# Kernel optimization log

Hardware: AMD Instinct MI355X
Metric: run time of the kernel (lower is better)

Reference implementation:

```python
import jax, jax.numpy as jnp
import numpy as np

B, S, D, H, L, C = 64, 2048, 64, 256, 2, 8  # batch, seq, input, hidden, layers, classes


def setup_inputs() -> dict:
    key = jax.random.key(0)
    ks = jax.random.split(key, 12)
    k = 1.0 / np.sqrt(H)  # torch LSTM/Linear init scale
    u = lambda kk, shape: jax.random.uniform(kk, shape, jnp.float32, -k, k)
    x = jax.random.normal(ks[0], (B, S, D), jnp.float32)
    lengths = jax.random.randint(ks[1], (B,), 1, S + 1).astype(jnp.int32)
    return {
        "x": x,
        "lengths": lengths,
        "Wih0": u(ks[2], (4 * H, D)),
        "Whh0": u(ks[3], (4 * H, H)),
        "bih0": u(ks[4], (4 * H,)),
        "bhh0": u(ks[5], (4 * H,)),
        "Wih1": u(ks[6], (4 * H, H)),
        "Whh1": u(ks[7], (4 * H, H)),
        "bih1": u(ks[8], (4 * H,)),
        "bhh1": u(ks[9], (4 * H,)),
        "Wfc": u(ks[10], (C, H)),
        "bfc": u(ks[11], (C,)),
    }


def _lstm_layer(x, Wih, Whh, bih, bhh):
    # x: [B,S,Din] -> h-sequence [B,S,H]; torch gate order i,f,g,o
    pre = jnp.einsum('bsd,gd->bsg', x, Wih) + bih + bhh  # [B,S,4H]
    Hh = Whh.shape[1]
    bsz = x.shape[0]

    def step(carry, p_t):
        h, c = carry
        gates = p_t + h @ Whh.T  # [B,4H]
        i, f, g, o = jnp.split(gates, 4, axis=-1)
        i = jax.nn.sigmoid(i)
        f = jax.nn.sigmoid(f)
        g = jnp.tanh(g)
        o = jax.nn.sigmoid(o)
        c = f * c + i * g
        h = o * jnp.tanh(c)
        return (h, c), h

    init = (jnp.zeros((bsz, Hh), x.dtype), jnp.zeros((bsz, Hh), x.dtype))
    _, hs = jax.lax.scan(step, init, jnp.swapaxes(pre, 0, 1))  # [S,B,H]
    return jnp.swapaxes(hs, 0, 1)


def reference(x, lengths, Wih0, Whh0, bih0, bhh0, Wih1, Whh1, bih1, bhh1, Wfc, bfc):
    h1 = _lstm_layer(x, Wih0, Whh0, bih0, bhh0)   # [B,S,H]
    h2 = _lstm_layer(h1, Wih1, Whh1, bih1, bhh1)  # [B,S,H]
    # pad_packed_sequence zeros outputs beyond each sequence's length
    valid = (jnp.arange(S)[None, :] < lengths[:, None])[..., None]  # [B,S,1]
    h2 = jnp.where(valid, h2, 0.0)
    emissions = jnp.einsum('bsh,ch->bsc', h2, Wfc) + bfc  # [B,S,C]
    return emissions
```

## Files before the change

kernel.cpp:

```cpp
#include <hip/hip_runtime.h>
#include <hip/hip_bf16.h>

#define BATCH 64
#define SEQ   2048
#define DIN   64
#define HID   256
#define NCLS  8

__device__ __forceinline__ float sigm(float x)  { return 1.0f / (1.0f + __expf(-x)); }
__device__ __forceinline__ float tanh_f(float x){ return 1.0f - 2.0f / (__expf(2.0f * x) + 1.0f); }

__global__ void init_out_kernel(float* __restrict__ out, const float* __restrict__ bfc) {
    int idx = blockIdx.x * blockDim.x + threadIdx.x;
    if (idx < BATCH * SEQ * NCLS) out[idx] = bfc[idx & 7];
}

__global__ void lstm_l0_kernel(
    const float* __restrict__ x,    const float* __restrict__ Wih0,
    const float* __restrict__ Whh0, const float* __restrict__ bih0,
    const float* __restrict__ bhh0, float* __restrict__ hist,
    int* __restrict__ flagsA)
{
    const int P   = blockIdx.x & 31;
    const int mem = blockIdx.x >> 5;
    const int tid = threadIdx.x;
    const int p   = tid >> 7;
    const int r   = tid & 127;
    const int row = (r >> 5) * 256 + mem * 32 + (r & 31);

    float w[40];
#pragma unroll
    for (int q = 0; q < 40; ++q) {
        int col = p * 40 + q;
        w[q] = (col < DIN) ? Wih0[row * DIN + col] : Whh0[row * HID + (col - DIN)];
    }
#pragma unroll
    for (int q = 0; q < 40; ++q) asm volatile("" : "+v"(w[q]));

    float biasv = 0.f;
    if (tid < 256) {
        int rr = tid & 127;
        int row2 = (rr >> 5) * 256 + mem * 32 + (rr & 31);
        biasv = bih0[row2] + bhh0[row2];
    }
    asm volatile("" : "+v"(biasv));
    float creg = 0.f;

    __shared__ __align__(16) float v[640];
    __shared__ float pbuf[2048];
    __shared__ float act[256];

    for (int t = 0; t < SEQ; ++t) {
        if (t > 0 && tid < 8) {
            while (__hip_atomic_load(&flagsA[P * 8 + tid], __ATOMIC_ACQUIRE,
                                     __HIP_MEMORY_SCOPE_AGENT) < t) {}
        }
        __syncthreads();
        if (tid < 640) {
            int n = (tid >= 320) ? 1 : 0;
            int j = tid - n * 320;
            int b = 2 * P + n;
            float val;
            if (j < DIN) {
                val = x[((size_t)b * SEQ + t) * DIN + j];
            } else {
                val = (t == 0) ? 0.f
                    : __hip_atomic_load(&hist[((size_t)(t - 1) * BATCH + b) * HID + (j - DIN)],
                                        __ATOMIC_RELAXED, __HIP_MEMORY_SCOPE_AGENT);
            }
            v[n * 320 + j] = val;
        }
        __syncthreads();

        float a0 = 0.f, a1 = 0.f;
#pragma unroll
        for (int qq = 0; qq < 10; ++qq) {
            float4 va = *(const float4*)&v[p * 40 + qq * 4];
            a0 = fmaf(w[qq * 4 + 0], va.x, a0);
            a0 = fmaf(w[qq * 4 + 1], va.y, a0);
            a0 = fmaf(w[qq * 4 + 2], va.z, a0);
            a0 = fmaf(w[qq * 4 + 3], va.w, a0);
            float4 vb = *(const float4*)&v[320 + p * 40 + qq * 4];
            a1 = fmaf(w[qq * 4 + 0], vb.x, a1);
            a1 = fmaf(w[qq * 4 + 1], vb.y, a1);
            a1 = fmaf(w[qq * 4 + 2], vb.z, a1);
            a1 = fmaf(w[qq * 4 + 3], vb.w, a1);
        }
        pbuf[p * 128 + r]        = a0;
        pbuf[1024 + p * 128 + r] = a1;
        __syncthreads();

        if (tid < 256) {
            int n = tid >> 7, rr = tid & 127;
            float s = biasv;
#pragma unroll
            for (int q = 0; q < 8; ++q) s += pbuf[n * 1024 + q * 128 + rr];
            act[n * 128 + rr] = ((rr >> 5) == 2) ? tanh_f(s) : sigm(s);
        }
        __syncthreads();

        if (tid < 64) {
            int n = tid >> 5, k = tid & 31, b = 2 * P + n;
            float iv = act[n * 128 + k],      fv = act[n * 128 + 32 + k];
            float gv = act[n * 128 + 64 + k], ov = act[n * 128 + 96 + k];
            creg = fv * creg + iv * gv;
            float h = ov * tanh_f(creg);
            __hip_atomic_store(&hist[((size_t)t * BATCH + b) * HID + mem * 32 + k],
                               h, __ATOMIC_RELAXED, __HIP_MEMORY_SCOPE_AGENT);
        }
        if (tid == 0) {
            __hip_atomic_store(&flagsA[P * 8 + mem], t + 1, __ATOMIC_RELEASE,
                               __HIP_MEMORY_SCOPE_AGENT);
        }
    }
}

__global__ void lstm_l1_kernel(
    const float* __restrict__ hist, const float* __restrict__ Wih1,
    const float* __restrict__ Whh1, const float* __restrict__ bih1,
    const float* __restrict__ bhh1, const float* __restrict__ Wfc,
    const float* __restrict__ bfc,  const int* __restrict__ lengths,
    float* __restrict__ out, float* __restrict__ xbuf, int* __restrict__ flagsB)
{
    const int g   = blockIdx.x & 15;
    const int mem = blockIdx.x >> 4;
    const int tid = threadIdx.x;
    const int p   = tid >> 6;
    const int r   = tid & 63;
    const int row = (r >> 4) * 256 + mem * 16 + (r & 15);

    float w[32];
#pragma unroll
    for (int q = 0; q < 32; ++q) {
        int col = p * 32 + q;
        w[q] = (col < HID) ? Wih1[row * HID + col] : Whh1[row * HID + (col - HID)];
    }
#pragma unroll
    for (int q = 0; q < 32; ++q) asm volatile("" : "+v"(w[q]));

    float biasv = 0.f;
    if (tid < 256) {
        int rr = tid & 63;
        int row2 = (rr >> 4) * 256 + mem * 16 + (rr & 15);
        biasv = bih1[row2] + bhh1[row2];
    }
    asm volatile("" : "+v"(biasv));
    float creg = 0.f;

    const int nf = mem & 3;
    const int c0 = (mem >> 2) * 2;
    float wfc = 0.f;
    if (tid < 512) wfc = Wfc[(c0 + (tid >> 8)) * HID + (tid & 255)];
    asm volatile("" : "+v"(wfc));
    const int  lenb = lengths[4 * g + nf];
    float bfcv = (tid < 2) ? bfc[c0 + tid] : 0.f;

    __shared__ __align__(16) float vbuf[2048];
    __shared__ float pbuf[4096];
    __shared__ float act[256];
    __shared__ float fcred[8];

    for (int t = 0; t < SEQ; ++t) {
        if (t > 0 && tid < 16) {
            while (__hip_atomic_load(&flagsB[g * 16 + tid], __ATOMIC_ACQUIRE,
                                     __HIP_MEMORY_SCOPE_AGENT) < t) {}
        }
        __syncthreads();
        {
            int n = tid >> 8, j = tid & 255, b = 4 * g + n;
            vbuf[n * 512 + j] = hist[((size_t)t * BATCH + b) * HID + j];
            float hv = (t == 0) ? 0.f
                : __hip_atomic_load(&xbuf[((size_t)b * 2 + ((t - 1) & 1)) * HID + j],
                                    __ATOMIC_RELAXED, __HIP_MEMORY_SCOPE_AGENT);
            vbuf[n * 512 + HID + j] = hv;
        }
        __syncthreads();

        float a0 = 0.f, a1 = 0.f, a2 = 0.f, a3 = 0.f;
#pragma unroll
        for (int qq = 0; qq < 8; ++qq) {
            float4 v0 = *(const float4*)&vbuf[p * 32 + qq * 4];
            a0 = fmaf(w[qq * 4 + 0], v0.x, a0); a0 = fmaf(w[qq * 4 + 1], v0.y, a0);
            a0 = fmaf(w[qq * 4 + 2], v0.z, a0); a0 = fmaf(w[qq * 4 + 3], v0.w, a0);
            float4 v1 = *(const float4*)&vbuf[512 + p * 32 + qq * 4];
            a1 = fmaf(w[qq * 4 + 0], v1.x, a1); a1 = fmaf(w[qq * 4 + 1], v1.y, a1);
            a1 = fmaf(w[qq * 4 + 2], v1.z, a1); a1 = fmaf(w[qq * 4 + 3], v1.w, a1);
            float4 v2 = *(const float4*)&vbuf[1024 + p * 32 + qq * 4];
            a2 = fmaf(w[qq * 4 + 0], v2.x, a2); a2 = fmaf(w[qq * 4 + 1], v2.y, a2);
            a2 = fmaf(w[qq * 4 + 2], v2.z, a2); a2 = fmaf(w[qq * 4 + 3], v2.w, a2);
            float4 v3 = *(const float4*)&vbuf[1536 + p * 32 + qq * 4];
            a3 = fmaf(w[qq * 4 + 0], v3.x, a3); a3 = fmaf(w[qq * 4 + 1], v3.y, a3);
            a3 = fmaf(w[qq * 4 + 2], v3.z, a3); a3 = fmaf(w[qq * 4 + 3], v3.w, a3);
        }
        pbuf[p * 64 + r]        = a0;
        pbuf[1024 + p * 64 + r] = a1;
        pbuf[2048 + p * 64 + r] = a2;
        pbuf[3072 + p * 64 + r] = a3;

        float fval = 0.f;
        if (t > 0 && tid < 512) {
            fval = vbuf[nf * 512 + HID + (tid & 255)] * wfc;
            fval += __shfl_xor(fval, 1);
            fval += __shfl_xor(fval, 2);
            fval += __shfl_xor(fval, 4);
            fval += __shfl_xor(fval, 8);
            fval += __shfl_xor(fval, 16);
            fval += __shfl_xor(fval, 32);
            if ((tid & 63) == 0) fcred[tid >> 6] = fval;
        }
        __syncthreads();

        if (tid < 256) {
            int n = tid >> 6, rw = tid & 63;
            float s = biasv;
#pragma unroll
            for (int q = 0; q < 16; ++q) s += pbuf[n * 1024 + q * 64 + rw];
            act[n * 64 + rw] = ((rw >> 4) == 2) ? tanh_f(s) : sigm(s);
        }
        if (t > 0 && tid < 2 && (t - 1) < lenb) {
            float s2 = fcred[tid * 4 + 0] + fcred[tid * 4 + 1]
                     + fcred[tid * 4 + 2] + fcred[tid * 4 + 3];
            out[((size_t)(4 * g + nf) * SEQ + (t - 1)) * NCLS + c0 + tid] = bfcv + s2;
        }
        __syncthreads();

        if (tid < 64) {
            int n = tid >> 4, k = tid & 15, b = 4 * g + n;
            float iv = act[n * 64 + k],      fv = act[n * 64 + 16 + k];
            float gv = act[n * 64 + 32 + k], ov = act[n * 64 + 48 + k];
            creg = fv * creg + iv * gv;
            float h = ov * tanh_f(creg);
            __hip_atomic_store(&xbuf[((size_t)b * 2 + (t & 1)) * HID + mem * 16 + k],
                               h, __ATOMIC_RELAXED, __HIP_MEMORY_SCOPE_AGENT);
        }
        if (tid == 0) {
            __hip_atomic_store(&flagsB[g * 16 + mem], t + 1, __ATOMIC_RELEASE,
                               __HIP_MEMORY_SCOPE_AGENT);
        }
    }

    if (tid < 16) {
        while (__hip_atomic_load(&flagsB[g * 16 + tid], __ATOMIC_ACQUIRE,
                                 __HIP_MEMORY_SCOPE_AGENT) < SEQ) {}
    }
    __syncthreads();
    float fval = 0.f;
    if (tid < 512) {
        int b = 4 * g + nf;
        float hv = __hip_atomic_load(&xbuf[((size_t)b * 2 + ((SEQ - 1) & 1)) * HID + (tid & 255)],
                                     __ATOMIC_RELAXED, __HIP_MEMORY_SCOPE_AGENT);
        fval = hv * wfc;
        fval += __shfl_xor(fval, 1);
        fval += __shfl_xor(fval, 2);
        fval += __shfl_xor(fval, 4);
        fval += __shfl_xor(fval, 8);
        fval += __shfl_xor(fval, 16);
        fval += __shfl_xor(fval, 32);
        if ((tid & 63) == 0) fcred[tid >> 6] = fval;
    }
    __syncthreads();
    if (tid < 2 && (SEQ - 1) < lenb) {
        float s2 = fcred[tid * 4 + 0] + fcred[tid * 4 + 1]
                 + fcred[tid * 4 + 2] + fcred[tid * 4 + 3];
        out[((size_t)(4 * g + nf) * SEQ + (SEQ - 1)) * NCLS + c0 + tid] = bfcv + s2;
    }
}

extern "C" void kernel_launch(void* const* d_in, const int* in_sizes, int n_in,
                              void* d_out, int out_size, void* d_ws, size_t ws_size,
                              hipStream_t stream) {
    (void)in_sizes; (void)n_in; (void)out_size;
    const float* x     = (const float*)d_in[0];
    const int*   lens  = (const int*)  d_in[1];
    const float* Wih0  = (const float*)d_in[2];
    const float* Whh0  = (const float*)d_in[3];
    const float* bih0  = (const float*)d_in[4];
    const float* bhh0  = (const float*)d_in[5];
    const float* Wih1  = (const float*)d_in[6];
    const float* Whh1  = (const float*)d_in[7];
    const float* bih1  = (const float*)d_in[8];
    const float* bhh1  = (const float*)d_in[9];
    const float* Wfc   = (const float*)d_in[10];
    const float* bfc   = (const float*)d_in[11];
    float* out = (float*)d_out;
    char*  ws  = (char*)d_ws;

    int*   flagsA = (int*)(ws);
    int*   flagsB = (int*)(ws + 1024);
    float* xbuf   = (float*)(ws + 2048);
    const size_t hist_off = 2048 + (size_t)BATCH * 2 * HID * 4;
    float* hist = (float*)(ws + hist_off);
    const size_t need = hist_off + (size_t)SEQ * BATCH * HID * 4;
    if (ws_size < need) return;

    hipMemsetAsync(ws, 0, hist_off, stream);
    init_out_kernel<<<(BATCH * SEQ * NCLS + 255) / 256, 256, 0, stream>>>(out, bfc);
    lstm_l0_kernel<<<256, 1024, 0, stream>>>(x, Wih0, Whh0, bih0, bhh0, hist, flagsA);
    lstm_l1_kernel<<<256, 1024, 0, stream>>>(hist, Wih1, Whh1, bih1, bhh1, Wfc, bfc,
                                             lens, out, xbuf, flagsB);
}
```

Measured before the change: 24.18 ms.

## Fuse both LSTM layers into one persistent kernel with wavefront pipelining

Result: slower. 30.66 ms (+26.8%).

```diff
diff --git a/kernel.cpp b/kernel.cpp
--- a/kernel.cpp
+++ b/kernel.cpp
@@ -10,196 +10,240 @@
 __device__ __forceinline__ float sigm(float x)  { return 1.0f / (1.0f + __expf(-x)); }
 __device__ __forceinline__ float tanh_f(float x){ return 1.0f - 2.0f / (__expf(2.0f * x) + 1.0f); }
 
+__device__ __forceinline__ void waitflag(int* f, int tgt) {
+    while (__hip_atomic_load(f, __ATOMIC_RELAXED, __HIP_MEMORY_SCOPE_AGENT) < tgt) {}
+    (void)__hip_atomic_load(f, __ATOMIC_ACQUIRE, __HIP_MEMORY_SCOPE_AGENT);
+}
+
 __global__ void init_out_kernel(float* __restrict__ out, const float* __restrict__ bfc) {
     int idx = blockIdx.x * blockDim.x + threadIdx.x;
     if (idx < BATCH * SEQ * NCLS) out[idx] = bfc[idx & 7];
 }
 
-__global__ void lstm_l0_kernel(
-    const float* __restrict__ x,    const float* __restrict__ Wih0,
-    const float* __restrict__ Whh0, const float* __restrict__ bih0,
-    const float* __restrict__ bhh0, float* __restrict__ hist,
-    int* __restrict__ flagsA)
+__global__ __launch_bounds__(1024) void lstm_fused_kernel(
+    const float* __restrict__ x,
+    const float* __restrict__ Wih0, const float* __restrict__ Whh0,
+    const float* __restrict__ bih0, const float* __restrict__ bhh0,
+    const float* __restrict__ Wih1, const float* __restrict__ Whh1,
+    const float* __restrict__ bih1, const float* __restrict__ bhh1,
+    const float* __restrict__ Wfc,  const float* __restrict__ bfc,
+    const int* __restrict__ lengths, float* __restrict__ out,
+    float* __restrict__ hist, float* __restrict__ xbuf,
+    int* __restrict__ flagsA, int* __restrict__ flagsB)
 {
-    const int P   = blockIdx.x & 31;
-    const int mem = blockIdx.x >> 5;
+    __shared__ __align__(16) float smem[6184];
     const int tid = threadIdx.x;
-    const int p   = tid >> 7;
-    const int r   = tid & 127;
-    const int row = (r >> 5) * 256 + mem * 32 + (r & 31);
-
-    float w[40];
-#pragma unroll
-    for (int q = 0; q < 40; ++q) {
-        int col = p * 40 + q;
-        w[q] = (col < DIN) ? Wih0[row * DIN + col] : Whh0[row * HID + (col - DIN)];
-    }
-#pragma unroll
-    for (int q = 0; q < 40; ++q) asm volatile("" : "+v"(w[q]));
-
-    float biasv = 0.f;
-    if (tid < 256) {
-        int rr = tid & 127;
-        int row2 = (rr >> 5) * 256 + mem * 32 + (rr & 31);
-        biasv = bih0[row2] + bhh0[row2];
-    }
-    asm volatile("" : "+v"(biasv));
-    float creg = 0.f;
-
-    __shared__ __align__(16) float v[640];
-    __shared__ float pbuf[2048];
-    __shared__ float act[256];
-
-    for (int t = 0; t < SEQ; ++t) {
-        if (t > 0 && tid < 8) {
-            while (__hip_atomic_load(&flagsA[P * 8 + tid], __ATOMIC_ACQUIRE,
-                                     __HIP_MEMORY_SCOPE_AGENT) < t) {}
-        }
+
+    if (blockIdx.x < 256) {
+        const int mem = blockIdx.x >> 5;
+        const int q   = blockIdx.x & 31;
+        const int P   = 2 * (q & 15) + (q >> 4);
+        const int p   = tid >> 7;
+        const int r   = tid & 127;
+        const int row = (r >> 5) * 256 + mem * 32 + (r & 31);
+
+        float w[40];
+#pragma unroll
+        for (int i = 0; i < 40; ++i) {
+            int col = p * 40 + i;
+            w[i] = (col < DIN) ? Wih0[row * DIN + col] : Whh0[row * HID + (col - DIN)];
+        }
+#pragma unroll
+        for (int i = 0; i < 40; ++i) asm volatile("" : "+v"(w[i]));
+
+        float bias4[4] = {0.f, 0.f, 0.f, 0.f};
+        if (tid < 64) {
+            int k = tid & 31;
+#pragma unroll
+            for (int g4 = 0; g4 < 4; ++g4) {
+                int rg = g4 * 256 + mem * 32 + k;
+                bias4[g4] = bih0[rg] + bhh0[rg];
+            }
+        }
+        float creg = 0.f;
+        float xreg = 0.f;
+        int   xn = 0, xj = 0;
+        if (tid >= 512 && tid < 640) {
+            xn = (tid - 512) >> 6; xj = tid & 63;
+            xreg = x[((size_t)(2 * P + xn) * SEQ) * DIN + xj];
+        }
+
+        float* v  = smem;
+        float* pb = smem + 640;
+
+        for (int t = 0; t < SEQ; ++t) {
+            if (t > 0 && tid < 8) waitflag(&flagsA[P * 8 + tid], t);
+            __syncthreads();
+            if (tid < 512) {
+                int n = tid >> 8, j = tid & 255, b = 2 * P + n;
+                v[n * 320 + 64 + j] = (t == 0) ? 0.f
+                    : hist[((size_t)(t - 1) * BATCH + b) * HID + j];
+            } else if (tid < 640) {
+                v[xn * 320 + xj] = xreg;
+            }
+            __syncthreads();
+            float a0 = 0.f, a1 = 0.f;
+#pragma unroll
+            for (int qq = 0; qq < 10; ++qq) {
+                float4 va = *(const float4*)&v[p * 40 + qq * 4];
+                a0 = fmaf(w[qq * 4 + 0], va.x, a0);
+                a0 = fmaf(w[qq * 4 + 1], va.y, a0);
+                a0 = fmaf(w[qq * 4 + 2], va.z, a0);
+                a0 = fmaf(w[qq * 4 + 3], va.w, a0);
+                float4 vb2 = *(const float4*)&v[320 + p * 40 + qq * 4];
+                a1 = fmaf(w[qq * 4 + 0], vb2.x, a1);
+                a1 = fmaf(w[qq * 4 + 1], vb2.y, a1);
+                a1 = fmaf(w[qq * 4 + 2], vb2.z, a1);
+                a1 = fmaf(w[qq * 4 + 3], vb2.w, a1);
+            }
+            pb[tid]        = a0;
+            pb[1024 + tid] = a1;
+            if (tid >= 512 && tid < 640 && t + 1 < SEQ) {
+                xreg = x[((size_t)(2 * P + xn) * SEQ + (t + 1)) * DIN + xj];
+            }
+            __syncthreads();
+            if (tid < 64) {
+                int n = tid >> 5, k = tid & 31, b = 2 * P + n;
+                float s0 = bias4[0], s1 = bias4[1], s2 = bias4[2], s3 = bias4[3];
+#pragma unroll
+                for (int q8 = 0; q8 < 8; ++q8) {
+                    int base = n * 1024 + q8 * 128 + k;
+                    s0 += pb[base];
+                    s1 += pb[base + 32];
+                    s2 += pb[base + 64];
+                    s3 += pb[base + 96];
+                }
+                float iv = sigm(s0), fv = sigm(s1), gv = tanh_f(s2), ov = sigm(s3);
+                creg = fv * creg + iv * gv;
+                float h = ov * tanh_f(creg);
+                hist[((size_t)t * BATCH + b) * HID + mem * 32 + k] = h;
+            }
+            if (tid == 0) {
+                __hip_atomic_store(&flagsA[P * 8 + mem], t + 1, __ATOMIC_RELEASE,
+                                   __HIP_MEMORY_SCOPE_AGENT);
+            }
+        }
+    } else {
+        const int bxx = blockIdx.x - 256;
+        const int mem = bxx >> 4;
+        const int g   = bxx & 15;
+        const int p   = tid >> 6;
+        const int r   = tid & 63;
+        const int row = (r >> 4) * 256 + mem * 16 + (r & 15);
+
+        float w[32];
+#pragma unroll
+        for (int i = 0; i < 32; ++i) {
+            int col = p * 32 + i;
+            w[i] = (col < HID) ? Wih1[row * HID + col] : Whh1[row * HID + (col - HID)];
+        }
+#pragma unroll
+        for (int i = 0; i < 32; ++i) asm volatile("" : "+v"(w[i]));
+
+        float bias4[4] = {0.f, 0.f, 0.f, 0.f};
+        if (tid < 64) {
+            int k = tid & 15;
+#pragma unroll
+            for (int g4 = 0; g4 < 4; ++g4) {
+                int rg = g4 * 256 + mem * 16 + k;
+                bias4[g4] = bih1[rg] + bhh1[rg];
+            }
+        }
+        const int nf = mem & 3;
+        const int c0 = (mem >> 2) * 2;
+        float wfc = 0.f;
+        if (tid < 512) wfc = Wfc[(c0 + (tid >> 8)) * HID + (tid & 255)];
+        asm volatile("" : "+v"(wfc));
+        const int   lenb = lengths[4 * g + nf];
+        const float bfc0 = bfc[c0], bfc1 = bfc[c0 + 1];
+        float creg = 0.f;
+
+        float* vb    = smem;
+        float* pb    = smem + 2048;
+        float* fcred = smem + 6176;
+
+        for (int t = 0; t < SEQ; ++t) {
+            if (tid < 16) {
+                int pi = tid >> 3, m = tid & 7;
+                waitflag(&flagsA[(2 * g + pi) * 8 + m], t + 1);
+            } else if (tid < 32 && t > 0) {
+                waitflag(&flagsB[g * 16 + (tid - 16)], t);
+            }
+            __syncthreads();
+            {
+                int n = tid >> 8, j = tid & 255, b = 4 * g + n;
+                vb[n * 512 + j] = hist[((size_t)t * BATCH + b) * HID + j];
+                vb[n * 512 + 256 + j] = (t == 0) ? 0.f
+                    : xbuf[((size_t)b * 2 + ((t - 1) & 1)) * HID + j];
+            }
+            __syncthreads();
+            float a0 = 0.f, a1 = 0.f, a2 = 0.f, a3 = 0.f;
+#pragma unroll
+            for (int qq = 0; qq < 8; ++qq) {
+                int base = p * 32 + qq * 4;
+                float4 v0 = *(const float4*)&vb[base];
+                a0 = fmaf(w[qq * 4 + 0], v0.x, a0); a0 = fmaf(w[qq * 4 + 1], v0.y, a0);
+                a0 = fmaf(w[qq * 4 + 2], v0.z, a0); a0 = fmaf(w[qq * 4 + 3], v0.w, a0);
+                float4 v1 = *(const float4*)&vb[512 + base];
+                a1 = fmaf(w[qq * 4 + 0], v1.x, a1); a1 = fmaf(w[qq * 4 + 1], v1.y, a1);
+                a1 = fmaf(w[qq * 4 + 2], v1.z, a1); a1 = fmaf(w[qq * 4 + 3], v1.w, a1);
+                float4 v2 = *(const float4*)&vb[1024 + base];
+                a2 = fmaf(w[qq * 4 + 0], v2.x, a2); a2 = fmaf(w[qq * 4 + 1], v2.y, a2);
+                a2 = fmaf(w[qq * 4 + 2], v2.z, a2); a2 = fmaf(w[qq * 4 + 3], v2.w, a2);
+                float4 v3 = *(const float4*)&vb[1536 + base];
+                a3 = fmaf(w[qq * 4 + 0], v3.x, a3); a3 = fmaf(w[qq * 4 + 1], v3.y, a3);
+                a3 = fmaf(w[qq * 4 + 2], v3.z, a3); a3 = fmaf(w[qq * 4 + 3], v3.w, a3);
+            }
+            pb[tid]            = a0;
+            pb[1032 + tid]     = a1;
+            pb[2064 + tid]     = a2;
+            pb[3096 + tid]     = a3;
+            float fval = 0.f;
+            if (t > 0 && tid < 512) {
+                fval = vb[nf * 512 + 256 + (tid & 255)] * wfc;
+                fval += __shfl_xor(fval, 1);
+                fval += __shfl_xor(fval, 2);
+                fval += __shfl_xor(fval, 4);
+                fval += __shfl_xor(fval, 8);
+                fval += __shfl_xor(fval, 16);
+                fval += __shfl_xor(fval, 32);
+                if ((tid & 63) == 0) fcred[tid >> 6] = fval;
+            }
+            __syncthreads();
+            if (tid < 64) {
+                int n = tid >> 4, k = tid & 15, b = 4 * g + n;
+                float s0 = bias4[0], s1 = bias4[1], s2 = bias4[2], s3 = bias4[3];
+#pragma unroll
+                for (int q16 = 0; q16 < 16; ++q16) {
+                    int base = n * 1032 + q16 * 64 + k;
+                    s0 += pb[base];
+                    s1 += pb[base + 16];
+                    s2 += pb[base + 32];
+                    s3 += pb[base + 48];
+                }
+                float iv = sigm(s0), fv = sigm(s1), gv = tanh_f(s2), ov = sigm(s3);
+                creg = fv * creg + iv * gv;
+                float h = ov * tanh_f(creg);
+                xbuf[((size_t)b * 2 + (t & 1)) * HID + mem * 16 + k] = h;
+            } else if (tid < 66 && t > 0 && (t - 1) < lenb) {
+                int cls = tid - 64;
+                float s2 = fcred[cls * 4 + 0] + fcred[cls * 4 + 1]
+                         + fcred[cls * 4 + 2] + fcred[cls * 4 + 3];
+                out[((size_t)(4 * g + nf) * SEQ + (t - 1)) * NCLS + c0 + cls]
+                    = (cls ? bfc1 : bfc0) + s2;
+            }
+            if (tid == 0) {
+                __hip_atomic_store(&flagsB[g * 16 + mem], t + 1, __ATOMIC_RELEASE,
+                                   __HIP_MEMORY_SCOPE_AGENT);
+            }
+        }
+        if (tid < 16) waitflag(&flagsB[g * 16 + tid], SEQ);
         __syncthreads();
-        if (tid < 640) {
-            int n = (tid >= 320) ? 1 : 0;
-            int j = tid - n * 320;
-            int b = 2 * P + n;
-            float val;
-            if (j < DIN) {
-                val = x[((size_t)b * SEQ + t) * DIN + j];
-            } else {
-                val = (t == 0) ? 0.f
-                    : __hip_atomic_load(&hist[((size_t)(t - 1) * BATCH + b) * HID + (j - DIN)],
-                                        __ATOMIC_RELAXED, __HIP_MEMORY_SCOPE_AGENT);
-            }
-            v[n * 320 + j] = val;
-        }
-        __syncthreads();
-
-        float a0 = 0.f, a1 = 0.f;
-#pragma unroll
-        for (int qq = 0; qq < 10; ++qq) {
-            float4 va = *(const float4*)&v[p * 40 + qq * 4];
-            a0 = fmaf(w[qq * 4 + 0], va.x, a0);
-            a0 = fmaf(w[qq * 4 + 1], va.y, a0);
-            a0 = fmaf(w[qq * 4 + 2], va.z, a0);
-            a0 = fmaf(w[qq * 4 + 3], va.w, a0);
-            float4 vb = *(const float4*)&v[320 + p * 40 + qq * 4];
-            a1 = fmaf(w[qq * 4 + 0], vb.x, a1);
-            a1 = fmaf(w[qq * 4 + 1], vb.y, a1);
-            a1 = fmaf(w[qq * 4 + 2], vb.z, a1);
-            a1 = fmaf(w[qq * 4 + 3], vb.w, a1);
-        }
-        pbuf[p * 128 + r]        = a0;
-        pbuf[1024 + p * 128 + r] = a1;
-        __syncthreads();
-
-        if (tid < 256) {
-            int n = tid >> 7, rr = tid & 127;
-            float s = biasv;
-#pragma unroll
-            for (int q = 0; q < 8; ++q) s += pbuf[n * 1024 + q * 128 + rr];
-            act[n * 128 + rr] = ((rr >> 5) == 2) ? tanh_f(s) : sigm(s);
-        }
-        __syncthreads();
-
-        if (tid < 64) {
-            int n = tid >> 5, k = tid & 31, b = 2 * P + n;
-            float iv = act[n * 128 + k],      fv = act[n * 128 + 32 + k];
-            float gv = act[n * 128 + 64 + k], ov = act[n * 128 + 96 + k];
-            creg = fv * creg + iv * gv;
-            float h = ov * tanh_f(creg);
-            __hip_atomic_store(&hist[((size_t)t * BATCH + b) * HID + mem * 32 + k],
-                               h, __ATOMIC_RELAXED, __HIP_MEMORY_SCOPE_AGENT);
-        }
-        if (tid == 0) {
-            __hip_atomic_store(&flagsA[P * 8 + mem], t + 1, __ATOMIC_RELEASE,
-                               __HIP_MEMORY_SCOPE_AGENT);
-        }
-    }
-}
-
-__global__ void lstm_l1_kernel(
-    const float* __restrict__ hist, const float* __restrict__ Wih1,
-    const float* __restrict__ Whh1, const float* __restrict__ bih1,
-    const float* __restrict__ bhh1, const float* __restrict__ Wfc,
-    const float* __restrict__ bfc,  const int* __restrict__ lengths,
-    float* __restrict__ out, float* __restrict__ xbuf, int* __restrict__ flagsB)
-{
-    const int g   = blockIdx.x & 15;
-    const int mem = blockIdx.x >> 4;
-    const int tid = threadIdx.x;
-    const int p   = tid >> 6;
-    const int r   = tid & 63;
-    const int row = (r >> 4) * 256 + mem * 16 + (r & 15);
-
-    float w[32];
-#pragma unroll
-    for (int q = 0; q < 32; ++q) {
-        int col = p * 32 + q;
-        w[q] = (col < HID) ? Wih1[row * HID + col] : Whh1[row * HID + (col - HID)];
-    }
-#pragma unroll
-    for (int q = 0; q < 32; ++q) asm volatile("" : "+v"(w[q]));
-
-    float biasv = 0.f;
-    if (tid < 256) {
-        int rr = tid & 63;
-        int row2 = (rr >> 4) * 256 + mem * 16 + (rr & 15);
-        biasv = bih1[row2] + bhh1[row2];
-    }
-    asm volatile("" : "+v"(biasv));
-    float creg = 0.f;
-
-    const int nf = mem & 3;
-    const int c0 = (mem >> 2) * 2;
-    float wfc = 0.f;
-    if (tid < 512) wfc = Wfc[(c0 + (tid >> 8)) * HID + (tid & 255)];
-    asm volatile("" : "+v"(wfc));
-    const int  lenb = lengths[4 * g + nf];
-    float bfcv = (tid < 2) ? bfc[c0 + tid] : 0.f;
-
-    __shared__ __align__(16) float vbuf[2048];
-    __shared__ float pbuf[4096];
-    __shared__ float act[256];
-    __shared__ float fcred[8];
-
-    for (int t = 0; t < SEQ; ++t) {
-        if (t > 0 && tid < 16) {
-            while (__hip_atomic_load(&flagsB[g * 16 + tid], __ATOMIC_ACQUIRE,
-                                     __HIP_MEMORY_SCOPE_AGENT) < t) {}
-        }
-        __syncthreads();
-        {
-            int n = tid >> 8, j = tid & 255, b = 4 * g + n;
-            vbuf[n * 512 + j] = hist[((size_t)t * BATCH + b) * HID + j];
-            float hv = (t == 0) ? 0.f
-                : __hip_atomic_load(&xbuf[((size_t)b * 2 + ((t - 1) & 1)) * HID + j],
-                                    __ATOMIC_RELAXED, __HIP_MEMORY_SCOPE_AGENT);
-            vbuf[n * 512 + HID + j] = hv;
-        }
-        __syncthreads();
-
-        float a0 = 0.f, a1 = 0.f, a2 = 0.f, a3 = 0.f;
-#pragma unroll
-        for (int qq = 0; qq < 8; ++qq) {
-            float4 v0 = *(const float4*)&vbuf[p * 32 + qq * 4];
-            a0 = fmaf(w[qq * 4 + 0], v0.x, a0); a0 = fmaf(w[qq * 4 + 1], v0.y, a0);
-            a0 = fmaf(w[qq * 4 + 2], v0.z, a0); a0 = fmaf(w[qq * 4 + 3], v0.w, a0);
-            float4 v1 = *(const float4*)&vbuf[512 + p * 32 + qq * 4];
-            a1 = fmaf(w[qq * 4 + 0], v1.x, a1); a1 = fmaf(w[qq * 4 + 1], v1.y, a1);
-            a1 = fmaf(w[qq * 4 + 2], v1.z, a1); a1 = fmaf(w[qq * 4 + 3], v1.w, a1);
-            float4 v2 = *(const float4*)&vbuf[1024 + p * 32 + qq * 4];
-            a2 = fmaf(w[qq * 4 + 0], v2.x, a2); a2 = fmaf(w[qq * 4 + 1], v2.y, a2);
-            a2 = fmaf(w[qq * 4 + 2], v2.z, a2); a2 = fmaf(w[qq * 4 + 3], v2.w, a2);
-            float4 v3 = *(const float4*)&vbuf[1536 + p * 32 + qq * 4];
-            a3 = fmaf(w[qq * 4 + 0], v3.x, a3); a3 = fmaf(w[qq * 4 + 1], v3.y, a3);
-            a3 = fmaf(w[qq * 4 + 2], v3.z, a3); a3 = fmaf(w[qq * 4 + 3], v3.w, a3);
-        }
-        pbuf[p * 64 + r]        = a0;
-        pbuf[1024 + p * 64 + r] = a1;
-        pbuf[2048 + p * 64 + r] = a2;
-        pbuf[3072 + p * 64 + r] = a3;
-
         float fval = 0.f;
-        if (t > 0 && tid < 512) {
-            fval = vbuf[nf * 512 + HID + (tid & 255)] * wfc;
+        if (tid < 512) {
+            int b = 4 * g + nf;
+            float hv = xbuf[((size_t)b * 2 + ((SEQ - 1) & 1)) * HID + (tid & 255)];
+            fval = hv * wfc;
             fval += __shfl_xor(fval, 1);
             fval += __shfl_xor(fval, 2);
             fval += __shfl_xor(fval, 4);
@@ -209,60 +253,12 @@
             if ((tid & 63) == 0) fcred[tid >> 6] = fval;
         }
         __syncthreads();
-
-        if (tid < 256) {
-            int n = tid >> 6, rw = tid & 63;
-            float s = biasv;
-#pragma unroll
-            for (int q = 0; q < 16; ++q) s += pbuf[n * 1024 + q * 64 + rw];
-            act[n * 64 + rw] = ((rw >> 4) == 2) ? tanh_f(s) : sigm(s);
-        }
-        if (t > 0 && tid < 2 && (t - 1) < lenb) {
+        if (tid < 2 && (SEQ - 1) < lenb) {
             float s2 = fcred[tid * 4 + 0] + fcred[tid * 4 + 1]
                      + fcred[tid * 4 + 2] + fcred[tid * 4 + 3];
-            out[((size_t)(4 * g + nf) * SEQ + (t - 1)) * NCLS + c0 + tid] = bfcv + s2;
-        }
-        __syncthreads();
-
-        if (tid < 64) {
-            int n = tid >> 4, k = tid & 15, b = 4 * g + n;
-            float iv = act[n * 64 + k],      fv = act[n * 64 + 16 + k];
-            float gv = act[n * 64 + 32 + k], ov = act[n * 64 + 48 + k];
-            creg = fv * creg + iv * gv;
-            float h = ov * tanh_f(creg);
-            __hip_atomic_store(&xbuf[((size_t)b * 2 + (t & 1)) * HID + mem * 16 + k],
-                               h, __ATOMIC_RELAXED, __HIP_MEMORY_SCOPE_AGENT);
-        }
-        if (tid == 0) {
-            __hip_atomic_store(&flagsB[g * 16 + mem], t + 1, __ATOMIC_RELEASE,
-                               __HIP_MEMORY_SCOPE_AGENT);
-        }
-    }
-
-    if (tid < 16) {
-        while (__hip_atomic_load(&flagsB[g * 16 + tid], __ATOMIC_ACQUIRE,
-                                 __HIP_MEMORY_SCOPE_AGENT) < SEQ) {}
-    }
-    __syncthreads();
-    float fval = 0.f;
-    if (tid < 512) {
-        int b = 4 * g + nf;
-        float hv = __hip_atomic_load(&xbuf[((size_t)b * 2 + ((SEQ - 1) & 1)) * HID + (tid & 255)],
-                                     __ATOMIC_RELAXED, __HIP_MEMORY_SCOPE_AGENT);
-        fval = hv * wfc;
-        fval += __shfl_xor(fval, 1);
-        fval += __shfl_xor(fval, 2);
-        fval += __shfl_xor(fval, 4);
-        fval += __shfl_xor(fval, 8);
-        fval += __shfl_xor(fval, 16);
-        fval += __shfl_xor(fval, 32);
-        if ((tid & 63) == 0) fcred[tid >> 6] = fval;
-    }
-    __syncthreads();
-    if (tid < 2 && (SEQ - 1) < lenb) {
-        float s2 = fcred[tid * 4 + 0] + fcred[tid * 4 + 1]
-                 + fcred[tid * 4 + 2] + fcred[tid * 4 + 3];
-        out[((size_t)(4 * g + nf) * SEQ + (SEQ - 1)) * NCLS + c0 + tid] = bfcv + s2;
+            out[((size_t)(4 * g + nf) * SEQ + (SEQ - 1)) * NCLS + c0 + tid]
+                = (tid ? bfc1 : bfc0) + s2;
+        }
     }
 }
 
@@ -293,9 +289,10 @@
     const size_t need = hist_off + (size_t)SEQ * BATCH * HID * 4;
     if (ws_size < need) return;
 
-    hipMemsetAsync(ws, 0, hist_off, stream);
+    hipMemsetAsync(ws, 0, 2048, stream);
     init_out_kernel<<<(BATCH * SEQ * NCLS + 255) / 256, 256, 0, stream>>>(out, bfc);
-    lstm_l0_kernel<<<256, 1024, 0, stream>>>(x, Wih0, Whh0, bih0, bhh0, hist, flagsA);
-    lstm_l1_kernel<<<256, 1024, 0, stream>>>(hist, Wih1, Whh1, bih1, bhh1, Wfc, bfc,
-                                             lens, out, xbuf, flagsB);
-}
+    lstm_fused_kernel<<<512, 1024, 0, stream>>>(x, Wih0, Whh0, bih0, bhh0,
+                                                Wih1, Whh1, bih1, bhh1,
+                                                Wfc, bfc, lens, out,
+                                                hist, xbuf, flagsA, flagsB);
+}
```
